# Kernel optimization log

Measured on AMD Instinct MI355X. Metric: run time of the kernel, lower is better.

Reference implementation:

```python
import jax, jax.numpy as jnp
import numpy as np
from jax import lax

EPS = 1e-5

def _groupnorm1(v, scale, bias):
    # GroupNorm(1, C) on [bs, C] vectors (spatial dims are 1x1): normalize over C per sample
    m = jnp.mean(v, axis=-1, keepdims=True)
    var = jnp.mean((v - m) ** 2, axis=-1, keepdims=True)
    return (v - m) / jnp.sqrt(var + EPS) * scale + bias

def _mish(v):
    return v * jnp.tanh(jax.nn.softplus(v))


def setup_inputs() -> dict:
    key = jax.random.key(0)
    ks = jax.random.split(key, 5)
    bs, C, H, W = 32, 128, 64, 64
    K, red = 4, 16
    hid = C // red
    return {
        "x": jax.random.normal(ks[0], (bs, C, H, W), jnp.float32),
        "weight": jax.random.normal(ks[1], (K, C, C, 3, 3), jnp.float32) * 0.05,
        "bias": jax.random.normal(ks[2], (K, C), jnp.float32) * 0.05,
        "se_w1": jax.random.normal(ks[3], (hid, C), jnp.float32) * 0.1,
        "gn1_scale": jnp.ones((hid,), jnp.float32),
        "gn1_bias": jnp.zeros((hid,), jnp.float32),
        "se_w2": jax.random.normal(ks[4], (K, hid), jnp.float32) * 0.1,
        "gn2_scale": jnp.ones((K,), jnp.float32),
        "gn2_bias": jnp.zeros((K,), jnp.float32),
    }


def reference(x, weight, bias, se_w1, gn1_scale, gn1_bias, se_w2, gn2_scale, gn2_bias):
    bs, C, H, W = x.shape
    K, out_p, in_p, kh, kw = weight.shape

    # --- SqueezeAndExcitation attention -> [bs, K] in (0,1) ---
    pooled = jnp.mean(x, axis=(2, 3))                       # [bs, C]
    h1 = pooled @ se_w1.T                                   # [bs, hid] (1x1 conv, no bias)
    h1 = _mish(_groupnorm1(h1, gn1_scale, gn1_bias))
    h2 = h1 @ se_w2.T                                       # [bs, K]
    att = jax.nn.sigmoid(_groupnorm1(h2, gn2_scale, gn2_bias))

    # --- per-sample kernel / bias aggregation ---
    agg_w = jnp.einsum('bk,koihw->boihw', att, weight)      # [bs, out, in, kh, kw]
    agg_b = att @ bias                                      # [bs, out]

    # --- per-sample conv2d (equivalent to groups=bs grouped conv in torch) ---
    pad = ((1, 1), (1, 1))
    def per_sample(xi, wi):
        return lax.conv_general_dilated(
            xi[None], wi, window_strides=(1, 1), padding=pad,
            dimension_numbers=('NCHW', 'OIHW', 'NCHW'))[0]
    out = jax.vmap(per_sample)(x, agg_w)                    # [bs, out, H, W]
    return out + agg_b[:, :, None, None]
```

## Files before the change

kernel.cpp:

```cpp
#include <hip/hip_runtime.h>
#include <hip/hip_bf16.h>
#include <math.h>
#include <stdint.h>

#define EPS 1e-5f

typedef __attribute__((ext_vector_type(8))) short bf16x8;
typedef __attribute__((ext_vector_type(16))) float f32x16;

__device__ __forceinline__ ushort f2bf(float f) {
    union { float f; unsigned u; } v; v.f = f;
    unsigned r = (v.u + 0x7FFFu + ((v.u >> 16) & 1u)) >> 16;
    return (ushort)r;
}

__device__ __forceinline__ void dma16(const void* g, void* l) {
    __builtin_amdgcn_global_load_lds(
        (__attribute__((address_space(1))) const void*)(uintptr_t)g,
        (__attribute__((address_space(3))) void*)(uintptr_t)l,
        16, 0, 0);
}

__global__ __launch_bounds__(256) void transpose_kernel(const float* __restrict__ x,
                                                        ushort* __restrict__ xT,
                                                        float* __restrict__ partial) {
    __shared__ float T[128][65];
    int bid = blockIdx.x;
    int b = (bid & 7) * 4 + (bid >> 9);
    int y = (bid >> 3) & 63;
    int t = threadIdx.x;

    int ic2 = t >> 1, half = t & 1;
    const float4* src = (const float4*)(x + (((size_t)b * 128 + ic2) * 64 + y) * 64 + half * 32);
    float s = 0.f;
#pragma unroll
    for (int i = 0; i < 8; ++i) {
        float4 v = src[i];
        int c0 = half * 32 + i * 4;
        T[ic2][c0] = v.x; T[ic2][c0 + 1] = v.y; T[ic2][c0 + 2] = v.z; T[ic2][c0 + 3] = v.w;
        s += v.x + v.y + v.z + v.w;
    }
    s += __shfl_xor(s, 1, 64);
    if (half == 0) partial[((size_t)b * 64 + y) * 128 + ic2] = s;
    __syncthreads();

    int col = t & 63, icq = t >> 6;
    uint pk[16];
#pragma unroll
    for (int j = 0; j < 16; ++j) {
        float f0 = T[icq * 32 + 2 * j][col];
        float f1 = T[icq * 32 + 2 * j + 1][col];
        pk[j] = (uint)f2bf(f0) | ((uint)f2bf(f1) << 16);
    }
    ushort* dst = xT + (((size_t)(b * 66 + y + 1)) * 66 + col + 1) * 128 + icq * 32;
    ((uint4*)dst)[0] = make_uint4(pk[0], pk[1], pk[2], pk[3]);
    ((uint4*)dst)[1] = make_uint4(pk[4], pk[5], pk[6], pk[7]);
    ((uint4*)dst)[2] = make_uint4(pk[8], pk[9], pk[10], pk[11]);
    ((uint4*)dst)[3] = make_uint4(pk[12], pk[13], pk[14], pk[15]);

    uint4 z = make_uint4(0, 0, 0, 0);
    if (y == 0) {
        uint4* row0 = (uint4*)(xT + ((size_t)b * 66 + 0) * 66 * 128);
        for (int i = t; i < 1056; i += 256) row0[i] = z;
    }
    if (y == 63) {
        uint4* row65 = (uint4*)(xT + ((size_t)b * 66 + 65) * 66 * 128);
        for (int i = t; i < 1056; i += 256) row65[i] = z;
    }
    if (t < 32) {
        int c = (t >> 4) * 65;
        int i = t & 15;
        *(uint4*)(xT + (((size_t)(b * 66 + y + 1)) * 66 + c) * 128 + i * 8) = z;
    }
}

__global__ __launch_bounds__(256) void sefuse_kernel(const float* __restrict__ partial,
                                                     const float* __restrict__ se_w1,
                                                     const float* __restrict__ gn1_s, const float* __restrict__ gn1_b,
                                                     const float* __restrict__ se_w2,
                                                     const float* __restrict__ gn2_s, const float* __restrict__ gn2_b,
                                                     float* __restrict__ att) {
    __shared__ float sA[256];
    __shared__ float pl[128];
    __shared__ float h1s[8];
    int b = blockIdx.x;
    int t = threadIdx.x;
    int ic = t & 127, hf = t >> 7;

    const float* p = partial + ((size_t)b * 64 + hf * 32) * 128 + ic;
    float s = 0.f;
#pragma unroll
    for (int k = 0; k < 32; ++k) s += p[k * 128];
    sA[t] = s;
    __syncthreads();
    if (t < 128) pl[t] = (sA[t] + sA[t + 128]) * (1.0f / 4096.0f);
    __syncthreads();
    if (t < 8) {
        float s1 = 0.f;
        for (int c = 0; c < 128; ++c) s1 += pl[c] * se_w1[t * 128 + c];
        h1s[t] = s1;
    }
    __syncthreads();
    if (t == 0) {
        float h1[8];
#pragma unroll
        for (int j = 0; j < 8; ++j) h1[j] = h1s[j];
        float m = 0.f;
#pragma unroll
        for (int j = 0; j < 8; ++j) m += h1[j];
        m *= 0.125f;
        float var = 0.f;
#pragma unroll
        for (int j = 0; j < 8; ++j) { float d = h1[j] - m; var += d * d; }
        var *= 0.125f;
        float inv = rsqrtf(var + EPS);
#pragma unroll
        for (int j = 0; j < 8; ++j) {
            float tt = (h1[j] - m) * inv * gn1_s[j] + gn1_b[j];
            float sp = (tt > 20.f) ? tt : log1pf(expf(tt));
            h1[j] = tt * tanhf(sp);
        }
        float h2[4];
#pragma unroll
        for (int k = 0; k < 4; ++k) {
            float s2 = 0.f;
#pragma unroll
            for (int j = 0; j < 8; ++j) s2 += h1[j] * se_w2[k * 8 + j];
            h2[k] = s2;
        }
        float m2 = 0.25f * (h2[0] + h2[1] + h2[2] + h2[3]);
        float v2 = 0.f;
#pragma unroll
        for (int k = 0; k < 4; ++k) { float d = h2[k] - m2; v2 += d * d; }
        v2 *= 0.25f;
        float inv2 = rsqrtf(v2 + EPS);
#pragma unroll
        for (int k = 0; k < 4; ++k) {
            float tt = (h2[k] - m2) * inv2 * gn2_s[k] + gn2_b[k];
            att[b * 4 + k] = 1.0f / (1.0f + expf(-tt));
        }
    }
}

__global__ __launch_bounds__(256) void aggw_kernel(const float* __restrict__ weight,
                                                   const float* __restrict__ att,
                                                   ushort* __restrict__ aggw) {
    int tq = (blockIdx.x % 72) * 256 + threadIdx.x;
    int rep = blockIdx.x / 72;
    int tap = tq >> 10;
    int within = tq & 1023;
    int oc = within >> 3;
    int p = within & 7;
    int g = (p - oc) & 7;
    int h = tap / 9, s = tap % 9;
    int ic0 = h * 64 + g * 8;

    float wv[4][8];
#pragma unroll
    for (int k = 0; k < 4; ++k)
#pragma unroll
        for (int j = 0; j < 8; ++j)
            wv[k][j] = weight[(((size_t)(k * 128 + oc)) * 128 + ic0 + j) * 9 + s];

    for (int b = rep * 8; b < rep * 8 + 8; ++b) {
        float a0 = att[b * 4 + 0], a1 = att[b * 4 + 1], a2 = att[b * 4 + 2], a3 = att[b * 4 + 3];
        uint pk[4];
#pragma unroll
        for (int q = 0; q < 4; ++q) {
            float f0 = a0 * wv[0][2 * q] + a1 * wv[1][2 * q] + a2 * wv[2][2 * q] + a3 * wv[3][2 * q];
            float f1 = a0 * wv[0][2 * q + 1] + a1 * wv[1][2 * q + 1] + a2 * wv[2][2 * q + 1] + a3 * wv[3][2 * q + 1];
            pk[q] = (uint)f2bf(f0) | ((uint)f2bf(f1) << 16);
        }
        *(uint4*)(aggw + (size_t)b * 147456 + (size_t)tq * 8) = make_uint4(pk[0], pk[1], pk[2], pk[3]);
    }
}

__global__ __launch_bounds__(256, 2) void conv_kernel(const ushort* __restrict__ xT,
                                                      const ushort* __restrict__ aggw,
                                                      const float* __restrict__ att,
                                                      const float* __restrict__ bias,
                                                      float* __restrict__ out) {
    __shared__ ushort ldsB[396 * 64];

    int bid = blockIdx.x;
    int xcd = bid & 7;
    int idx = bid >> 3;
    int b = xcd * 4 + (idx >> 4);
    int tile = idx & 15;
    int y0 = tile * 4;

    int tid = threadIdx.x;
    int l = tid & 63, w = tid >> 6;
    int wm = w >> 1, wn = w & 1;
    int l31 = l & 31, lhi = l >> 5;

    const ushort* xTb = xT + ((size_t)(b * 66 + y0)) * 66 * 128;
    const ushort* Asmp = aggw + (size_t)b * 147456;

    const ushort* ptrA[2];
    int rotA[2];
#pragma unroll
    for (int mi = 0; mi < 2; ++mi) {
        int oc = wm * 64 + mi * 32 + l31;
        ptrA[mi] = Asmp + oc * 64;
        rotA[mi] = (lhi + oc) & 7;
    }
    int CB[4];
#pragma unroll
    for (int nb = 0; nb < 4; ++nb) {
        int rs = nb >> 1, ch = nb & 1;
        CB[nb] = (2 * wn + rs) * 66 + ch * 32 + l31;
    }
    int rotB = (l31 + lhi) & 7;

    f32x16 acc[2][4];
#pragma unroll
    for (int mi = 0; mi < 2; ++mi)
#pragma unroll
        for (int nb = 0; nb < 4; ++nb)
#pragma unroll
            for (int q = 0; q < 16; ++q) acc[mi][nb][q] = 0.f;

    bf16x8 a[2][4];
#pragma unroll
    for (int mi = 0; mi < 2; ++mi)
#pragma unroll
        for (int icb = 0; icb < 4; ++icb)
            a[mi][icb] = *(const bf16x8*)(ptrA[mi] + (((rotA[mi] + 2 * icb) & 7) << 3));

#pragma unroll
    for (int i = 0; i < 13; ++i) {
        int k = i * 256 + tid;
        if (k < 3168) {
            int rc = k >> 3;
            int c = rc % 66;
            int g = ((k & 7) - c) & 7;
            dma16(xTb + (size_t)rc * 128 + (g << 3), &ldsB[(size_t)k * 8]);
        }
    }
    __syncthreads();

    for (int hs = 0; hs < 18; ++hs) {
        int s = (hs >= 9) ? hs - 9 : hs;
        int kh = s / 3, kw = s - kh * 3;
        int celladd = kh * 66 + kw;
        const ushort* Anext = Asmp + (size_t)(hs + 1) * 8192;
#pragma unroll
        for (int icb = 0; icb < 4; ++icb) {
            int slotb = (rotB + 2 * icb + kw) & 7;
            bf16x8 bb[4];
#pragma unroll
            for (int nb = 0; nb < 4; ++nb) {
                int cell = CB[nb] + celladd;
                bb[nb] = *(const bf16x8*)&ldsB[(cell << 6) + (slotb << 3)];
            }
#pragma unroll
            for (int mi = 0; mi < 2; ++mi)
#pragma unroll
                for (int nb = 0; nb < 4; ++nb)
                    acc[mi][nb] = __builtin_amdgcn_mfma_f32_32x32x16_bf16(a[mi][icb], bb[nb], acc[mi][nb], 0, 0, 0);
            if (hs < 17) {
#pragma unroll
                for (int mi = 0; mi < 2; ++mi) {
                    int oc64 = (wm * 64 + mi * 32 + l31) * 64;
                    a[mi][icb] = *(const bf16x8*)(Anext + oc64 + (((rotA[mi] + 2 * icb) & 7) << 3));
                }
            }
        }
        if (hs == 8) {
            __syncthreads();
#pragma unroll
            for (int i = 0; i < 13; ++i) {
                int k = i * 256 + tid;
                if (k < 3168) {
                    int rc = k >> 3;
                    int c = rc % 66;
                    int g = ((k & 7) - c) & 7;
                    dma16(xTb + (size_t)rc * 128 + 64 + (g << 3), &ldsB[(size_t)k * 8]);
                }
            }
            __syncthreads();
        }
    }

    float a0 = att[b * 4 + 0], a1 = att[b * 4 + 1], a2 = att[b * 4 + 2], a3 = att[b * 4 + 3];
#pragma unroll
    for (int mi = 0; mi < 2; ++mi)
#pragma unroll
        for (int q = 0; q < 16; ++q) {
            int oc = wm * 64 + mi * 32 + (q & 3) + 8 * (q >> 2) + 4 * lhi;
            float ab = a0 * bias[oc] + a1 * bias[128 + oc] + a2 * bias[256 + oc] + a3 * bias[384 + oc];
#pragma unroll
            for (int nb = 0; nb < 4; ++nb) {
                int y = y0 + 2 * wn + (nb >> 1);
                out[(((size_t)b * 128 + oc) * 64 + y) * 64 + (nb & 1) * 32 + l31] = acc[mi][nb][q] + ab;
            }
        }
}

extern "C" void kernel_launch(void* const* d_in, const int* in_sizes, int n_in,
                              void* d_out, int out_size, void* d_ws, size_t ws_size,
                              hipStream_t stream) {
    const float* x      = (const float*)d_in[0];
    const float* weight = (const float*)d_in[1];
    const float* bias   = (const float*)d_in[2];
    const float* se_w1  = (const float*)d_in[3];
    const float* gn1_s  = (const float*)d_in[4];
    const float* gn1_b  = (const float*)d_in[5];
    const float* se_w2  = (const float*)d_in[6];
    const float* gn2_s  = (const float*)d_in[7];
    const float* gn2_b  = (const float*)d_in[8];
    float* out = (float*)d_out;

    float*  att     = (float*)((char*)d_ws + 16384);
    float*  partial = (float*)((char*)d_ws + 65536);
    ushort* aggw    = (ushort*)((char*)d_ws + 65536);
    ushort* xT      = (ushort*)((char*)d_ws + 10485760);

    transpose_kernel<<<2048, 256, 0, stream>>>(x, xT, partial);
    sefuse_kernel<<<32, 256, 0, stream>>>(partial, se_w1, gn1_s, gn1_b, se_w2, gn2_s, gn2_b, att);
    aggw_kernel<<<288, 256, 0, stream>>>(weight, att, aggw);
    conv_kernel<<<512, 256, 0, stream>>>(xT, aggw, att, bias, out);
}
```

Before: 88.95 us.

## Double conv waves per block and transpose LDS layout for vectorized reads

```diff
diff --git a/kernel.cpp b/kernel.cpp
--- a/kernel.cpp
+++ b/kernel.cpp
@@ -24,7 +24,7 @@
 __global__ __launch_bounds__(256) void transpose_kernel(const float* __restrict__ x,
                                                         ushort* __restrict__ xT,
                                                         float* __restrict__ partial) {
-    __shared__ float T[128][65];
+    __shared__ float T2[64][132];
     int bid = blockIdx.x;
     int b = (bid & 7) * 4 + (bid >> 9);
     int y = (bid >> 3) & 63;
@@ -37,20 +37,21 @@
     for (int i = 0; i < 8; ++i) {
         float4 v = src[i];
         int c0 = half * 32 + i * 4;
-        T[ic2][c0] = v.x; T[ic2][c0 + 1] = v.y; T[ic2][c0 + 2] = v.z; T[ic2][c0 + 3] = v.w;
+        T2[c0][ic2] = v.x; T2[c0 + 1][ic2] = v.y; T2[c0 + 2][ic2] = v.z; T2[c0 + 3][ic2] = v.w;
         s += v.x + v.y + v.z + v.w;
     }
     s += __shfl_xor(s, 1, 64);
     if (half == 0) partial[((size_t)b * 64 + y) * 128 + ic2] = s;
     __syncthreads();
 
-    int col = t & 63, icq = t >> 6;
+    int col = t >> 2, icq = t & 3;
+    const float4* row = (const float4*)&T2[col][icq * 32];
     uint pk[16];
 #pragma unroll
-    for (int j = 0; j < 16; ++j) {
-        float f0 = T[icq * 32 + 2 * j][col];
-        float f1 = T[icq * 32 + 2 * j + 1][col];
-        pk[j] = (uint)f2bf(f0) | ((uint)f2bf(f1) << 16);
+    for (int m = 0; m < 8; ++m) {
+        float4 v = row[m];
+        pk[2 * m]     = (uint)f2bf(v.x) | ((uint)f2bf(v.y) << 16);
+        pk[2 * m + 1] = (uint)f2bf(v.z) | ((uint)f2bf(v.w) << 16);
     }
     ushort* dst = xT + (((size_t)(b * 66 + y + 1)) * 66 + col + 1) * 128 + icq * 32;
     ((uint4*)dst)[0] = make_uint4(pk[0], pk[1], pk[2], pk[3]);
@@ -175,7 +176,7 @@
     }
 }
 
-__global__ __launch_bounds__(256, 2) void conv_kernel(const ushort* __restrict__ xT,
+__global__ __launch_bounds__(512, 4) void conv_kernel(const ushort* __restrict__ xT,
                                                       const ushort* __restrict__ aggw,
                                                       const float* __restrict__ att,
                                                       const float* __restrict__ bias,
@@ -191,46 +192,42 @@
 
     int tid = threadIdx.x;
     int l = tid & 63, w = tid >> 6;
-    int wm = w >> 1, wn = w & 1;
+    int wm = w & 1, wn = w >> 1;
     int l31 = l & 31, lhi = l >> 5;
 
     const ushort* xTb = xT + ((size_t)(b * 66 + y0)) * 66 * 128;
     const ushort* Asmp = aggw + (size_t)b * 147456;
 
-    const ushort* ptrA[2];
-    int rotA[2];
+    int ocofs[2], rotA[2];
 #pragma unroll
     for (int mi = 0; mi < 2; ++mi) {
         int oc = wm * 64 + mi * 32 + l31;
-        ptrA[mi] = Asmp + oc * 64;
+        ocofs[mi] = oc * 64;
         rotA[mi] = (lhi + oc) & 7;
     }
-    int CB[4];
-#pragma unroll
-    for (int nb = 0; nb < 4; ++nb) {
-        int rs = nb >> 1, ch = nb & 1;
-        CB[nb] = (2 * wn + rs) * 66 + ch * 32 + l31;
-    }
+    int CB[2];
+#pragma unroll
+    for (int ch = 0; ch < 2; ++ch) CB[ch] = wn * 66 + ch * 32 + l31;
     int rotB = (l31 + lhi) & 7;
 
-    f32x16 acc[2][4];
+    f32x16 acc[2][2];
 #pragma unroll
     for (int mi = 0; mi < 2; ++mi)
 #pragma unroll
-        for (int nb = 0; nb < 4; ++nb)
-#pragma unroll
-            for (int q = 0; q < 16; ++q) acc[mi][nb][q] = 0.f;
+        for (int ch = 0; ch < 2; ++ch)
+#pragma unroll
+            for (int q = 0; q < 16; ++q) acc[mi][ch][q] = 0.f;
 
     bf16x8 a[2][4];
 #pragma unroll
     for (int mi = 0; mi < 2; ++mi)
 #pragma unroll
         for (int icb = 0; icb < 4; ++icb)
-            a[mi][icb] = *(const bf16x8*)(ptrA[mi] + (((rotA[mi] + 2 * icb) & 7) << 3));
-
-#pragma unroll
-    for (int i = 0; i < 13; ++i) {
-        int k = i * 256 + tid;
+            a[mi][icb] = *(const bf16x8*)(Asmp + ocofs[mi] + (((rotA[mi] + 2 * icb) & 7) << 3));
+
+#pragma unroll
+    for (int i = 0; i < 7; ++i) {
+        int k = i * 512 + tid;
         if (k < 3168) {
             int rc = k >> 3;
             int c = rc % 66;
@@ -248,30 +245,28 @@
 #pragma unroll
         for (int icb = 0; icb < 4; ++icb) {
             int slotb = (rotB + 2 * icb + kw) & 7;
-            bf16x8 bb[4];
-#pragma unroll
-            for (int nb = 0; nb < 4; ++nb) {
-                int cell = CB[nb] + celladd;
-                bb[nb] = *(const bf16x8*)&ldsB[(cell << 6) + (slotb << 3)];
+            bf16x8 bb[2];
+#pragma unroll
+            for (int ch = 0; ch < 2; ++ch) {
+                int cell = CB[ch] + celladd;
+                bb[ch] = *(const bf16x8*)&ldsB[(cell << 6) + (slotb << 3)];
             }
 #pragma unroll
             for (int mi = 0; mi < 2; ++mi)
 #pragma unroll
-                for (int nb = 0; nb < 4; ++nb)
-                    acc[mi][nb] = __builtin_amdgcn_mfma_f32_32x32x16_bf16(a[mi][icb], bb[nb], acc[mi][nb], 0, 0, 0);
+                for (int ch = 0; ch < 2; ++ch)
+                    acc[mi][ch] = __builtin_amdgcn_mfma_f32_32x32x16_bf16(a[mi][icb], bb[ch], acc[mi][ch], 0, 0, 0);
             if (hs < 17) {
 #pragma unroll
-                for (int mi = 0; mi < 2; ++mi) {
-                    int oc64 = (wm * 64 + mi * 32 + l31) * 64;
-                    a[mi][icb] = *(const bf16x8*)(Anext + oc64 + (((rotA[mi] + 2 * icb) & 7) << 3));
-                }
+                for (int mi = 0; mi < 2; ++mi)
+                    a[mi][icb] = *(const bf16x8*)(Anext + ocofs[mi] + (((rotA[mi] + 2 * icb) & 7) << 3));
             }
         }
         if (hs == 8) {
             __syncthreads();
 #pragma unroll
-            for (int i = 0; i < 13; ++i) {
-                int k = i * 256 + tid;
+            for (int i = 0; i < 7; ++i) {
+                int k = i * 512 + tid;
                 if (k < 3168) {
                     int rc = k >> 3;
                     int c = rc % 66;
@@ -284,6 +279,7 @@
     }
 
     float a0 = att[b * 4 + 0], a1 = att[b * 4 + 1], a2 = att[b * 4 + 2], a3 = att[b * 4 + 3];
+    int y = y0 + wn;
 #pragma unroll
     for (int mi = 0; mi < 2; ++mi)
 #pragma unroll
@@ -291,10 +287,8 @@
             int oc = wm * 64 + mi * 32 + (q & 3) + 8 * (q >> 2) + 4 * lhi;
             float ab = a0 * bias[oc] + a1 * bias[128 + oc] + a2 * bias[256 + oc] + a3 * bias[384 + oc];
 #pragma unroll
-            for (int nb = 0; nb < 4; ++nb) {
-                int y = y0 + 2 * wn + (nb >> 1);
-                out[(((size_t)b * 128 + oc) * 64 + y) * 64 + (nb & 1) * 32 + l31] = acc[mi][nb][q] + ab;
-            }
+            for (int ch = 0; ch < 2; ++ch)
+                out[(((size_t)b * 128 + oc) * 64 + y) * 64 + ch * 32 + l31] = acc[mi][ch][q] + ab;
         }
 }
 
@@ -320,5 +314,5 @@
     transpose_kernel<<<2048, 256, 0, stream>>>(x, xT, partial);
     sefuse_kernel<<<32, 256, 0, stream>>>(partial, se_w1, gn1_s, gn1_b, se_w2, gn2_s, gn2_b, att);
     aggw_kernel<<<288, 256, 0, stream>>>(weight, att, aggw);
-    conv_kernel<<<512, 256, 0, stream>>>(xT, aggw, att, bias, out);
-}
+    conv_kernel<<<512, 512, 0, stream>>>(xT, aggw, att, bias, out);
+}
```

Result: slower. 105.0 us (+18.0%).

## Double-buffer conv input staging in 32-channel chunks and rework LDS swizzle

Applied to the files above, without the earlier changes.

```diff
diff --git a/kernel.cpp b/kernel.cpp
--- a/kernel.cpp
+++ b/kernel.cpp
@@ -24,7 +24,7 @@
 __global__ __launch_bounds__(256) void transpose_kernel(const float* __restrict__ x,
                                                         ushort* __restrict__ xT,
                                                         float* __restrict__ partial) {
-    __shared__ float T[128][65];
+    __shared__ float T2[64][132];
     int bid = blockIdx.x;
     int b = (bid & 7) * 4 + (bid >> 9);
     int y = (bid >> 3) & 63;
@@ -37,20 +37,21 @@
     for (int i = 0; i < 8; ++i) {
         float4 v = src[i];
         int c0 = half * 32 + i * 4;
-        T[ic2][c0] = v.x; T[ic2][c0 + 1] = v.y; T[ic2][c0 + 2] = v.z; T[ic2][c0 + 3] = v.w;
+        T2[c0][ic2] = v.x; T2[c0 + 1][ic2] = v.y; T2[c0 + 2][ic2] = v.z; T2[c0 + 3][ic2] = v.w;
         s += v.x + v.y + v.z + v.w;
     }
     s += __shfl_xor(s, 1, 64);
     if (half == 0) partial[((size_t)b * 64 + y) * 128 + ic2] = s;
     __syncthreads();
 
-    int col = t & 63, icq = t >> 6;
+    int col = t >> 2, icq = t & 3;
+    const float4* row = (const float4*)&T2[col][icq * 32];
     uint pk[16];
 #pragma unroll
-    for (int j = 0; j < 16; ++j) {
-        float f0 = T[icq * 32 + 2 * j][col];
-        float f1 = T[icq * 32 + 2 * j + 1][col];
-        pk[j] = (uint)f2bf(f0) | ((uint)f2bf(f1) << 16);
+    for (int m = 0; m < 8; ++m) {
+        float4 v = row[m];
+        pk[2 * m]     = (uint)f2bf(v.x) | ((uint)f2bf(v.y) << 16);
+        pk[2 * m + 1] = (uint)f2bf(v.z) | ((uint)f2bf(v.w) << 16);
     }
     ushort* dst = xT + (((size_t)(b * 66 + y + 1)) * 66 + col + 1) * 128 + icq * 32;
     ((uint4*)dst)[0] = make_uint4(pk[0], pk[1], pk[2], pk[3]);
@@ -180,7 +181,7 @@
                                                       const float* __restrict__ att,
                                                       const float* __restrict__ bias,
                                                       float* __restrict__ out) {
-    __shared__ ushort ldsB[396 * 64];
+    __shared__ ushort ldsB[2][12672];
 
     int bid = blockIdx.x;
     int xcd = bid & 7;
@@ -197,21 +198,13 @@
     const ushort* xTb = xT + ((size_t)(b * 66 + y0)) * 66 * 128;
     const ushort* Asmp = aggw + (size_t)b * 147456;
 
-    const ushort* ptrA[2];
-    int rotA[2];
+    int ocofs[2], rotA[2];
 #pragma unroll
     for (int mi = 0; mi < 2; ++mi) {
         int oc = wm * 64 + mi * 32 + l31;
-        ptrA[mi] = Asmp + oc * 64;
+        ocofs[mi] = oc * 64;
         rotA[mi] = (lhi + oc) & 7;
     }
-    int CB[4];
-#pragma unroll
-    for (int nb = 0; nb < 4; ++nb) {
-        int rs = nb >> 1, ch = nb & 1;
-        CB[nb] = (2 * wn + rs) * 66 + ch * 32 + l31;
-    }
-    int rotB = (l31 + lhi) & 7;
 
     f32x16 acc[2][4];
 #pragma unroll
@@ -221,66 +214,90 @@
 #pragma unroll
             for (int q = 0; q < 16; ++q) acc[mi][nb][q] = 0.f;
 
-    bf16x8 a[2][4];
-#pragma unroll
-    for (int mi = 0; mi < 2; ++mi)
-#pragma unroll
-        for (int icb = 0; icb < 4; ++icb)
-            a[mi][icb] = *(const bf16x8*)(ptrA[mi] + (((rotA[mi] + 2 * icb) & 7) << 3));
-
-#pragma unroll
-    for (int i = 0; i < 13; ++i) {
-        int k = i * 256 + tid;
-        if (k < 3168) {
-            int rc = k >> 3;
-            int c = rc % 66;
-            int g = ((k & 7) - c) & 7;
-            dma16(xTb + (size_t)rc * 128 + (g << 3), &ldsB[(size_t)k * 8]);
-        }
-    }
-    __syncthreads();
-
-    for (int hs = 0; hs < 18; ++hs) {
-        int s = (hs >= 9) ? hs - 9 : hs;
-        int kh = s / 3, kw = s - kh * 3;
-        int celladd = kh * 66 + kw;
-        const ushort* Anext = Asmp + (size_t)(hs + 1) * 8192;
-#pragma unroll
-        for (int icb = 0; icb < 4; ++icb) {
-            int slotb = (rotB + 2 * icb + kw) & 7;
-            bf16x8 bb[4];
-#pragma unroll
-            for (int nb = 0; nb < 4; ++nb) {
-                int cell = CB[nb] + celladd;
-                bb[nb] = *(const bf16x8*)&ldsB[(cell << 6) + (slotb << 3)];
+    bf16x8 aR[3][2][2];
+
+#define LOADA(R, Q, S)                                                                       \
+    {                                                                                        \
+        const ushort* tb_ = Asmp + (size_t)((((Q) >> 1) * 9 + (S))) * 8192;                  \
+        _Pragma("unroll")                                                                    \
+        for (int ib_ = 0; ib_ < 2; ++ib_)                                                    \
+            _Pragma("unroll")                                                                \
+            for (int mi_ = 0; mi_ < 2; ++mi_)                                                \
+                aR[R][ib_][mi_] = *(const bf16x8*)(tb_ + ocofs[mi_] +                        \
+                    (((rotA[mi_] + 4 * ((Q) & 1) + 2 * ib_) & 7) << 3));                     \
+    }
+
+#define STAGE(Q, BUF)                                                                        \
+    {                                                                                        \
+        _Pragma("unroll")                                                                    \
+        for (int i_ = 0; i_ < 7; ++i_) {                                                     \
+            int k_ = i_ * 256 + tid;                                                         \
+            if (k_ < 1584) {                                                                 \
+                int rc_ = k_ >> 2;                                                           \
+                int p_ = k_ & 3;                                                             \
+                int c_ = rc_ % 66;                                                           \
+                int g_ = (p_ - c_ - (c_ >> 2)) & 3;                                          \
+                dma16(xTb + (size_t)rc_ * 128 + (Q) * 32 + (g_ << 3),                        \
+                      &ldsB[BUF][(size_t)k_ * 8]);                                           \
+            }                                                                                \
+        }                                                                                    \
+    }
+
+    STAGE(0, 0);
+    LOADA(0, 0, 0);
+    LOADA(1, 0, 1);
+    __syncthreads();
+
+    for (int q = 0; q < 4; ++q) {
+        int cur = q & 1;
+        if (q < 3) {
+            if (cur) { STAGE(q + 1, 0); } else { STAGE(q + 1, 1); }
+        }
+        const ushort* buf = ldsB[cur];
+#pragma unroll
+        for (int s = 0; s < 9; ++s) {
+            const int kh = s / 3, kw = s - kh * 3;
+            {
+                bf16x8 bb[4];
+#pragma unroll
+                for (int nb = 0; nb < 4; ++nb) {
+                    int r = 2 * wn + (nb >> 1) + kh;
+                    int c = (nb & 1) * 32 + l31 + kw;
+                    int p = (lhi + c + (c >> 2)) & 3;
+                    bb[nb] = *(const bf16x8*)&buf[((r * 66 + c) << 5) + (p << 3)];
+                }
+                __builtin_amdgcn_s_setprio(1);
+#pragma unroll
+                for (int mi = 0; mi < 2; ++mi)
+#pragma unroll
+                    for (int nb = 0; nb < 4; ++nb)
+                        acc[mi][nb] = __builtin_amdgcn_mfma_f32_32x32x16_bf16(aR[s % 3][0][mi], bb[nb], acc[mi][nb], 0, 0, 0);
+                __builtin_amdgcn_s_setprio(0);
             }
-#pragma unroll
-            for (int mi = 0; mi < 2; ++mi)
-#pragma unroll
-                for (int nb = 0; nb < 4; ++nb)
-                    acc[mi][nb] = __builtin_amdgcn_mfma_f32_32x32x16_bf16(a[mi][icb], bb[nb], acc[mi][nb], 0, 0, 0);
-            if (hs < 17) {
-#pragma unroll
-                for (int mi = 0; mi < 2; ++mi) {
-                    int oc64 = (wm * 64 + mi * 32 + l31) * 64;
-                    a[mi][icb] = *(const bf16x8*)(Anext + oc64 + (((rotA[mi] + 2 * icb) & 7) << 3));
+            if (q < 3 || s < 7) {
+                if (s < 7) { LOADA((s + 2) % 3, q, s + 2); }
+                else if (s == 7) { LOADA(0, q + 1, 0); }
+                else { LOADA(1, q + 1, 1); }
+            }
+            {
+                bf16x8 bb[4];
+#pragma unroll
+                for (int nb = 0; nb < 4; ++nb) {
+                    int r = 2 * wn + (nb >> 1) + kh;
+                    int c = (nb & 1) * 32 + l31 + kw;
+                    int p = (2 + lhi + c + (c >> 2)) & 3;
+                    bb[nb] = *(const bf16x8*)&buf[((r * 66 + c) << 5) + (p << 3)];
                 }
+                __builtin_amdgcn_s_setprio(1);
+#pragma unroll
+                for (int mi = 0; mi < 2; ++mi)
+#pragma unroll
+                    for (int nb = 0; nb < 4; ++nb)
+                        acc[mi][nb] = __builtin_amdgcn_mfma_f32_32x32x16_bf16(aR[s % 3][1][mi], bb[nb], acc[mi][nb], 0, 0, 0);
+                __builtin_amdgcn_s_setprio(0);
             }
         }
-        if (hs == 8) {
-            __syncthreads();
-#pragma unroll
-            for (int i = 0; i < 13; ++i) {
-                int k = i * 256 + tid;
-                if (k < 3168) {
-                    int rc = k >> 3;
-                    int c = rc % 66;
-                    int g = ((k & 7) - c) & 7;
-                    dma16(xTb + (size_t)rc * 128 + 64 + (g << 3), &ldsB[(size_t)k * 8]);
-                }
-            }
-            __syncthreads();
-        }
+        __syncthreads();
     }
 
     float a0 = att[b * 4 + 0], a1 = att[b * 4 + 1], a2 = att[b * 4 + 2], a3 = att[b * 4 + 3];
@@ -296,6 +313,8 @@
                 out[(((size_t)b * 128 + oc) * 64 + y) * 64 + (nb & 1) * 32 + l31] = acc[mi][nb][q] + ab;
             }
         }
+#undef LOADA
+#undef STAGE
 }
 
 extern "C" void kernel_launch(void* const* d_in, const int* in_sizes, int n_in,
```

New measurement: 102.4 us. +15.2%, slower.
